# Optimization experiments

Hardware: AMD Instinct MI355X
Metric: run time of the kernel (lower is better)

Reference implementation:

```python
import jax, jax.numpy as jnp
import numpy as np
import math

B, S, D = 1, 2048, 2048          # batch, seq_len, hidden_size
H, HD = 16, 128                  # attention heads, head_dim
HV, R, NV, K = 4, 128, 2048, 4   # inner value heads, retrieval dim, num_inner_values, values per head


def rotate_half(x):
    x1, x2 = x[..., :x.shape[-1] // 2], x[..., x.shape[-1] // 2:]
    return jnp.concatenate((-x2, x1), axis=-1)


def setup_inputs() -> dict:
    key = jax.random.key(0)
    ks = jax.random.split(key, 8)
    hidden_states = jax.random.normal(ks[0], (B, S, D), jnp.float32)
    attention_mask = jnp.ones((B, S), jnp.float32)
    # standard RoPE tables, shape [B, S, HD]
    inv_freq = 1.0 / (10000.0 ** (jnp.arange(0, HD, 2, dtype=jnp.float32) / HD))
    freqs = jnp.outer(jnp.arange(S, dtype=jnp.float32), inv_freq)
    emb = jnp.concatenate((freqs, freqs), axis=-1)
    cos = jnp.broadcast_to(jnp.cos(emb)[None], (B, S, HD))
    sin = jnp.broadcast_to(jnp.sin(emb)[None], (B, S, HD))
    # learned per-head dynamic mask (binary, like torch.round init)
    dynamic_mask = jnp.round(jax.random.uniform(ks[1], (H, S), jnp.float32))
    sc = 0.02
    Wq = jax.random.normal(ks[2], (D, D), jnp.float32) * sc
    Wk = jax.random.normal(ks[3], (D, D), jnp.float32) * sc
    Wvq = jax.random.normal(ks[4], (D, HV * R), jnp.float32) * sc
    v_keys = jax.random.normal(ks[5], (HV, R, NV), jnp.float32) * sc
    v_embed = jax.random.normal(ks[6], (NV, D), jnp.float32) * sc
    Wo = jax.random.normal(ks[7], (D, D), jnp.float32) * sc
    return dict(hidden_states=hidden_states, attention_mask=attention_mask,
                cos=cos, sin=sin, dynamic_mask=dynamic_mask,
                Wq=Wq, Wk=Wk, Wvq=Wvq, v_keys=v_keys, v_embed=v_embed, Wo=Wo)


def reference(hidden_states, attention_mask, cos, sin, dynamic_mask,
              Wq, Wk, Wvq, v_keys, v_embed, Wo):
    b, s, d = hidden_states.shape
    q = hidden_states @ Wq
    k = hidden_states @ Wk
    # ---- inner_func: product-key style value retrieval ----
    vq = (hidden_states @ Wvq).reshape(b, s, HV, R).transpose(0, 2, 1, 3)  # [b,HV,s,R]
    sim = jnp.einsum('bhsr,hrn->bhsn', vq, v_keys)                         # [b,HV,s,NV]
    _, idx = jax.lax.top_k(sim, K)                                         # [b,HV,s,K]
    ve = v_embed[idx]                                                      # [b,HV,s,K,d]
    v = hidden_states * ve.sum(axis=3).sum(axis=1)                         # [b,s,d]
    # ---- heads ----
    q = q.reshape(b, s, H, HD).transpose(0, 2, 1, 3)
    k = k.reshape(b, s, H, HD).transpose(0, 2, 1, 3)
    v = v.reshape(b, s, H, HD).transpose(0, 2, 1, 3)
    # NOTE: original code rotates ONLY q (k is never rotated) -- kept faithfully
    cu, su = cos[:, None], sin[:, None]                                    # [b,1,s,HD]
    q = q * cu + rotate_half(q) * su
    attn = jnp.einsum('bhqd,bhkd->bhqk', q, k) / math.sqrt(HD)
    # ---- causal mask fused with per-head dynamic mask ----
    min_v = jnp.finfo(attn.dtype).min
    i = jnp.arange(s)
    causal = jnp.where(i[None, :] > i[:, None], min_v, 0.0).astype(attn.dtype)   # [s,s]
    causal = jnp.broadcast_to(causal[None, None], (b, H, s, s))
    am = attention_mask[:, None, None, :] * dynamic_mask[None, :, None, :s]      # [b,H,1,s]
    mask = jnp.where(causal + am == 0, min_v, causal)
    p = jax.nn.softmax(attn + mask, axis=-1)
    out = jnp.einsum('bhqk,bhkd->bhqd', p, v)
    out = out.transpose(0, 2, 1, 3).reshape(b, s, d)
    return out @ Wo
```

## Files before the change

kernel.cpp:

```cpp
#include <hip/hip_runtime.h>
#include <float.h>

#define NEG_MIN (-3.4028234663852886e38f)
#define INV_SQRT_HD 0.08838834764831845f
#define SCALE_L2E 0.12751791437968458f

typedef __attribute__((ext_vector_type(8))) short bf16x8;
typedef __attribute__((ext_vector_type(8))) unsigned short u16x8;
typedef __attribute__((ext_vector_type(4))) float f32x4;

__device__ __forceinline__ void gload_lds16(const void* g, void* l) {
  __builtin_amdgcn_global_load_lds((const __attribute__((address_space(1))) void*)g,
                                   (__attribute__((address_space(3))) void*)l, 16, 0, 0);
}
__device__ __forceinline__ ushort f2bf(float x) {
  union { float f; unsigned u; } v; v.f = x;
  unsigned r = v.u + 0x7fffu + ((v.u >> 16) & 1u);
  return (ushort)(r >> 16);
}
__device__ __forceinline__ float bf2f(ushort u) {
  union { unsigned i; float f; } v; v.i = ((unsigned)u) << 16; return v.f;
}
template<int CTRL>
__device__ __forceinline__ float dpp_ror(float x) {
  return __int_as_float(__builtin_amdgcn_mov_dpp(__float_as_int(x), CTRL, 0xF, 0xF, true));
}
template<int CTRL>
__device__ __forceinline__ unsigned dpp_ror_u(unsigned x) {
  return (unsigned)__builtin_amdgcn_mov_dpp((int)x, CTRL, 0xF, 0xF, true);
}
__device__ __forceinline__ unsigned wave_umax64(unsigned x) {
  x = max(x, dpp_ror_u<0x121>(x));
  x = max(x, dpp_ror_u<0x122>(x));
  x = max(x, dpp_ror_u<0x124>(x));
  x = max(x, dpp_ror_u<0x128>(x));
  x = max(x, (unsigned)__shfl_xor((int)x, 16));
  x = max(x, (unsigned)__shfl_xor((int)x, 32));
  return x;
}
__device__ __forceinline__ unsigned bf_sortable(ushort b) {
  return (b & 0x8000u) ? (unsigned)(b ^ 0xFFFFu) : (unsigned)(b | 0x8000u);
}

__global__ __launch_bounds__(256) void gemm_f32_sk(
    const float* __restrict__ A, int lda,
    const float* __restrict__ B, int ldb,
    float* __restrict__ Cp, int ldc, int M, int N, int Kchunk)
{
  __shared__ float As[16][132];
  __shared__ float Bs[16][132];
  const int t = threadIdx.x, tx = t & 15, ty = t >> 4;
  const int bm = blockIdx.y << 7, bn = blockIdx.x << 7;
  const int k0base = blockIdx.z * Kchunk;
  const int arr = t >> 2, ac = (t & 3) << 2;
  const int brr = t >> 5, bc = (t & 31) << 2;

  float acc[8][8];
#pragma unroll
  for (int i = 0; i < 8; ++i)
#pragma unroll
    for (int j = 0; j < 8; ++j) acc[i][j] = 0.f;

  float4 pa0, pa1, pb0, pb1;
  pa0 = *(const float4*)(A + (size_t)(bm + arr) * lda + k0base + ac);
  pa1 = *(const float4*)(A + (size_t)(bm + arr + 64) * lda + k0base + ac);
  pb0 = *(const float4*)(B + (size_t)(k0base + brr) * ldb + bn + bc);
  pb1 = *(const float4*)(B + (size_t)(k0base + brr + 8) * ldb + bn + bc);

  for (int k0 = 0; k0 < Kchunk; k0 += 16) {
    __syncthreads();
    As[ac + 0][arr] = pa0.x; As[ac + 1][arr] = pa0.y;
    As[ac + 2][arr] = pa0.z; As[ac + 3][arr] = pa0.w;
    As[ac + 0][arr + 64] = pa1.x; As[ac + 1][arr + 64] = pa1.y;
    As[ac + 2][arr + 64] = pa1.z; As[ac + 3][arr + 64] = pa1.w;
    *(float4*)(&Bs[brr][bc])     = pb0;
    *(float4*)(&Bs[brr + 8][bc]) = pb1;
    __syncthreads();
    if (k0 + 16 < Kchunk) {
      int kn = k0base + k0 + 16;
      pa0 = *(const float4*)(A + (size_t)(bm + arr) * lda + kn + ac);
      pa1 = *(const float4*)(A + (size_t)(bm + arr + 64) * lda + kn + ac);
      pb0 = *(const float4*)(B + (size_t)(kn + brr) * ldb + bn + bc);
      pb1 = *(const float4*)(B + (size_t)(kn + brr + 8) * ldb + bn + bc);
    }
#pragma unroll
    for (int kk = 0; kk < 16; ++kk) {
      float4 a0 = *(const float4*)(&As[kk][ty * 8]);
      float4 a1 = *(const float4*)(&As[kk][ty * 8 + 4]);
      float4 b0 = *(const float4*)(&Bs[kk][tx * 4]);
      float4 b1 = *(const float4*)(&Bs[kk][tx * 4 + 64]);
      float av[8] = {a0.x, a0.y, a0.z, a0.w, a1.x, a1.y, a1.z, a1.w};
      float bv[8] = {b0.x, b0.y, b0.z, b0.w, b1.x, b1.y, b1.z, b1.w};
#pragma unroll
      for (int i = 0; i < 8; ++i)
#pragma unroll
        for (int j = 0; j < 8; ++j)
          acc[i][j] = fmaf(av[i], bv[j], acc[i][j]);
    }
  }
  float* C = Cp + (size_t)blockIdx.z * M * N;
#pragma unroll
  for (int i = 0; i < 8; ++i) {
    int row = bm + ty * 8 + i;
    *(float4*)(C + (size_t)row * ldc + bn + tx * 4) =
        make_float4(acc[i][0], acc[i][1], acc[i][2], acc[i][3]);
    *(float4*)(C + (size_t)row * ldc + bn + tx * 4 + 64) =
        make_float4(acc[i][4], acc[i][5], acc[i][6], acc[i][7]);
  }
}

__global__ __launch_bounds__(256) void reduce16_cvt(const float* __restrict__ Cp,
    float* __restrict__ vq, ushort* __restrict__ vq_bf)
{
  int i = (blockIdx.x * 256 + threadIdx.x) << 2;
  float4 s = make_float4(0.f, 0.f, 0.f, 0.f);
#pragma unroll
  for (int z = 0; z < 16; ++z) {
    float4 a = *(const float4*)(Cp + (size_t)z * 1048576 + i);
    s.x += a.x; s.y += a.y; s.z += a.z; s.w += a.w;
  }
  *(float4*)(vq + i) = s;
  ushort4 o; o.x = f2bf(s.x); o.y = f2bf(s.y); o.z = f2bf(s.z); o.w = f2bf(s.w);
  *(ushort4*)(vq_bf + i) = o;
}

template<int OUT_BF16, int ROPE>
__global__ __launch_bounds__(256) void gemm_bf16(
    const ushort* __restrict__ A0, int lda,
    const ushort* __restrict__ Bt0, int ldb,
    void* __restrict__ C0, int ldc, int Kd,
    size_t strA, size_t strB, size_t strC,
    const float* __restrict__ cosb, const float* __restrict__ sinb)
{
  const ushort* A  = A0  + blockIdx.z * strA;
  const ushort* Bt = Bt0 + blockIdx.z * strB;
  __shared__ ushort smem_g[2 * 128 * 64];
  ushort* As = smem_g;
  ushort* Bs = smem_g + 128 * 64;
  const int t = threadIdx.x, w = t >> 6, lane = t & 63;
  const int lr = lane & 15, lk = lane >> 4;
  const int bm = blockIdx.y << 7, bn = blockIdx.x << 7;
  const int wm = (w >> 1) << 6, wn = (w & 1) << 6;
  f32x4 acc[4][4];
#pragma unroll
  for (int i = 0; i < 4; ++i)
#pragma unroll
    for (int j = 0; j < 4; ++j) acc[i][j] = (f32x4){0.f, 0.f, 0.f, 0.f};

  for (int k0 = 0; k0 < Kd; k0 += 64) {
    __syncthreads();
#pragma unroll
    for (int qI = 0; qI < 4; ++qI) {
      int b = w * 4096 + qI * 1024 + lane * 16;
      int row = b >> 7, colb = b & 127;
      int src = colb ^ ((row & 7) << 4);
      gload_lds16((const char*)A + ((size_t)(bm + row) * lda + k0) * 2 + src,
                  (char*)As + w * 4096 + qI * 1024);
    }
#pragma unroll
    for (int qI = 0; qI < 4; ++qI) {
      int b = w * 4096 + qI * 1024 + lane * 16;
      int row = b >> 7, colb = b & 127;
      int src = colb ^ ((row & 7) << 4);
      gload_lds16((const char*)Bt + ((size_t)(bn + row) * ldb + k0) * 2 + src,
                  (char*)Bs + w * 4096 + qI * 1024);
    }
    __syncthreads();
#pragma unroll
    for (int kk = 0; kk < 2; ++kk) {
      bf16x8 af[4], bf[4];
#pragma unroll
      for (int mi = 0; mi < 4; ++mi) {
        int row = wm + mi * 16 + lr;
        af[mi] = *(const bf16x8*)((const char*)As + row * 128 + ((kk * 64 + lk * 16) ^ ((row & 7) << 4)));
      }
#pragma unroll
      for (int ni = 0; ni < 4; ++ni) {
        int row = wn + ni * 16 + lr;
        bf[ni] = *(const bf16x8*)((const char*)Bs + row * 128 + ((kk * 64 + lk * 16) ^ ((row & 7) << 4)));
      }
#pragma unroll
      for (int mi = 0; mi < 4; ++mi)
#pragma unroll
        for (int ni = 0; ni < 4; ++ni)
          acc[mi][ni] = __builtin_amdgcn_mfma_f32_16x16x32_bf16(af[mi], bf[ni], acc[mi][ni], 0, 0, 0);
    }
  }

  if (ROPE && blockIdx.x < 16) {
    __syncthreads();
    ushort* Pl = smem_g;
#pragma unroll
    for (int mi = 0; mi < 4; ++mi)
#pragma unroll
      for (int j = 0; j < 4; ++j) {
        int rl = wm + mi * 16 + lk * 4 + j;
#pragma unroll
        for (int ni = 0; ni < 4; ++ni)
          Pl[rl * 128 + wn + ni * 16 + lr] = f2bf(acc[mi][ni][j]);
      }
    __syncthreads();
    const bool lo = (wn == 0);
#pragma unroll
    for (int mi = 0; mi < 4; ++mi)
#pragma unroll
      for (int j = 0; j < 4; ++j) {
        int rl = wm + mi * 16 + lk * 4 + j;
        int row = bm + rl;
#pragma unroll
        for (int ni = 0; ni < 4; ++ni) {
          int d = wn + ni * 16 + lr;
          float a = bf2f(Pl[rl * 128 + d]);
          float b = bf2f(Pl[rl * 128 + (d ^ 64)]);
          float cs = cosb[row * 128 + d], sn = sinb[row * 128 + d];
          float v = lo ? (a * cs - b * sn) : (a * cs + b * sn);
          ((ushort*)C0)[(size_t)row * ldc + bn + d] = f2bf(v);
        }
      }
    return;
  }

#pragma unroll
  for (int mi = 0; mi < 4; ++mi)
#pragma unroll
    for (int j = 0; j < 4; ++j) {
      int row = bm + wm + mi * 16 + lk * 4 + j;
#pragma unroll
      for (int ni = 0; ni < 4; ++ni) {
        int col = bn + wn + ni * 16 + lr;
        if (OUT_BF16) ((ushort*)C0)[blockIdx.z * strC + (size_t)row * ldc + col] = f2bf(acc[mi][ni][j]);
        else          ((float*)C0)[blockIdx.z * strC + (size_t)row * ldc + col]  = acc[mi][ni][j];
      }
    }
}

__global__ __launch_bounds__(256) void transpose_cvt_vk(
    const float* __restrict__ src0, ushort* __restrict__ dstb,
    float* __restrict__ dstf)
{
  const float* src = src0 + (size_t)blockIdx.z * 262144;
  ushort* db = dstb + (size_t)blockIdx.z * 262144;
  float*  df = dstf + (size_t)blockIdx.z * 262144;
  __shared__ float tile[64][65];
  const int r0 = blockIdx.y << 6, c0 = blockIdx.x << 6;
  const int t = threadIdx.x;
  for (int i = t; i < 1024; i += 256) {
    int r = i >> 4, c = (i & 15) << 2;
    float4 v = *(const float4*)(src + (size_t)(r0 + r) * 2048 + c0 + c);
    tile[r][c] = v.x; tile[r][c+1] = v.y; tile[r][c+2] = v.z; tile[r][c+3] = v.w;
  }
  __syncthreads();
  int c = t >> 2, rb = (t & 3) << 4;
#pragma unroll
  for (int u = 0; u < 16; u += 4) {
    float4 f = make_float4(tile[rb+u+0][c], tile[rb+u+1][c],
                           tile[rb+u+2][c], tile[rb+u+3][c]);
    ushort4 o; o.x = f2bf(f.x); o.y = f2bf(f.y); o.z = f2bf(f.z); o.w = f2bf(f.w);
    *(ushort4*)(db + (size_t)(c0 + c) * 128 + r0 + rb + u) = o;
    *(float4*) (df + (size_t)(c0 + c) * 128 + r0 + rb + u) = f;
  }
}

__global__ __launch_bounds__(256) void transpose_cvt_w3(
    const float* __restrict__ srcA, const float* __restrict__ srcB,
    const float* __restrict__ srcC, ushort* __restrict__ dst0)
{
  const float* src = (blockIdx.z == 0) ? srcA : (blockIdx.z == 1) ? srcB : srcC;
  ushort* dst = dst0 + (size_t)blockIdx.z * 4194304;
  __shared__ float tile[64][65];
  const int r0 = blockIdx.y << 6, c0 = blockIdx.x << 6;
  const int t = threadIdx.x;
  for (int i = t; i < 1024; i += 256) {
    int r = i >> 4, c = (i & 15) << 2;
    float4 v = *(const float4*)(src + (size_t)(r0 + r) * 2048 + c0 + c);
    tile[r][c] = v.x; tile[r][c+1] = v.y; tile[r][c+2] = v.z; tile[r][c+3] = v.w;
  }
  __syncthreads();
  int c = t >> 2, rb = (t & 3) << 4;
#pragma unroll
  for (int u = 0; u < 16; u += 4) {
    ushort4 o;
    o.x = f2bf(tile[rb+u+0][c]); o.y = f2bf(tile[rb+u+1][c]);
    o.z = f2bf(tile[rb+u+2][c]); o.w = f2bf(tile[rb+u+3][c]);
    *(ushort4*)(dst + (size_t)(c0 + c) * 2048 + r0 + rb + u) = o;
  }
}

__global__ __launch_bounds__(256) void transpose_bf(
    const ushort* __restrict__ src, ushort* __restrict__ dst)
{
  __shared__ ushort tile[64][66];
  const int r0 = blockIdx.y << 6, c0 = blockIdx.x << 6;
  const int t = threadIdx.x;
  for (int i = t; i < 512; i += 256) {
    int r = i >> 3, c8 = (i & 7) << 3;
    *(u16x8*)(&tile[r][c8]) = *(const u16x8*)(src + (size_t)(r0 + r) * 2048 + c0 + c8);
  }
  __syncthreads();
  for (int i = t; i < 512; i += 256) {
    int c = i >> 3, r8 = (i & 7) << 3;
    u16x8 o;
#pragma unroll
    for (int u = 0; u < 8; ++u) o[u] = tile[r8 + u][c];
    *(u16x8*)(dst + (size_t)(c0 + c) * 2048 + r0 + r8) = o;
  }
}

__global__ __launch_bounds__(256) void cvt2_bf16(const float* __restrict__ srcA,
    ushort* __restrict__ dstA, const float* __restrict__ srcB,
    ushort* __restrict__ dstB)
{
  int gid = blockIdx.x * 256 + threadIdx.x;
  const float* s; ushort* d; int i;
  if (gid < 1048576) { s = srcA; d = dstA; i = gid; }
  else               { s = srcB; d = dstB; i = gid - 1048576; }
  float4 v = ((const float4*)s)[i];
  ushort4 o; o.x = f2bf(v.x); o.y = f2bf(v.y); o.z = f2bf(v.z); o.w = f2bf(v.w);
  ((ushort4*)d)[i] = o;
}

__global__ __launch_bounds__(256) void topk_sel(const ushort* __restrict__ sim,
    const float* __restrict__ vq, const float* __restrict__ vkTf,
    int* __restrict__ idxo)
{
  const int row = blockIdx.x * 4 + (threadIdx.x >> 6);
  const int hv = row >> 11, s = row & 2047;
  const int lane = threadIdx.x & 63;
  const ushort* r = sim + (size_t)row * 2048;

  unsigned v[8];
#pragma unroll
  for (int p = 0; p < 8; ++p) v[p] = 0u;
  for (int j = 0; j < 4; ++j) {
    int nb = (lane + (j << 6)) << 3;
    u16x8 e = *(const u16x8*)(r + nb);
#pragma unroll
    for (int u = 0; u < 8; ++u) {
      unsigned pk = (bf_sortable(e[u]) << 16) | (unsigned)(2047 - (nb + u));
      if (pk > v[7]) {
        v[7] = pk;
#pragma unroll
        for (int p = 7; p > 0; --p)
          if (v[p] > v[p-1]) { unsigned tt = v[p]; v[p] = v[p-1]; v[p-1] = tt; }
      }
    }
  }
  int out_n[8];
#pragma unroll
  for (int r8 = 0; r8 < 8; ++r8) {
    unsigned m = wave_umax64(v[0]);
    out_n[r8] = 2047 - (int)(m & 0x7FFu);
    if (v[0] == m) {
#pragma unroll
      for (int p = 0; p < 7; ++p) v[p] = v[p+1];
      v[7] = 0u;
    }
  }
  const int c = lane & 7, rc = lane >> 3;
  int n = 0;
#pragma unroll
  for (int p = 0; p < 8; ++p) if (p == c) n = out_n[p];
  const float* vqr = vq + (size_t)s * 512 + hv * 128 + rc * 16;
  const float* vkf = vkTf + (size_t)hv * 262144 + (size_t)n * 128 + rc * 16;
  float acc = 0.f;
#pragma unroll
  for (int u = 0; u < 16; ++u) acc = fmaf(vqr[u], vkf[u], acc);
  acc += __shfl_xor(acc, 8);
  acc += __shfl_xor(acc, 16);
  acc += __shfl_xor(acc, 32);
  float cv = acc; int ci = n;
  int picks[4];
#pragma unroll
  for (int p = 0; p < 4; ++p) {
    float bv = cv; int bi = ci;
#pragma unroll
    for (int d = 1; d < 8; d <<= 1) {
      float ov = __shfl_xor(bv, d); int oi = __shfl_xor(bi, d);
      if (ov > bv || (ov == bv && oi < bi)) { bv = ov; bi = oi; }
    }
    picks[p] = bi;
    if (bi == ci) cv = -FLT_MAX;
  }
  if (lane == 0) {
#pragma unroll
    for (int p = 0; p < 4; ++p) idxo[(size_t)row * 4 + p] = picks[p];
  }
}

__global__ __launch_bounds__(256) void gather_mul_bf(const float* __restrict__ hs,
    const ushort* __restrict__ vemb_bf, const int* __restrict__ idx,
    ushort* __restrict__ vb)
{
  const int s = blockIdx.x;
  const int t = threadIdx.x;
  __shared__ int id[16];
  if (t < 16) id[t] = idx[((size_t)(t >> 2) * 2048 + s) * 4 + (t & 3)];
  __syncthreads();
  int d0 = t << 3;
  float g[8] = {0.f, 0.f, 0.f, 0.f, 0.f, 0.f, 0.f, 0.f};
#pragma unroll
  for (int e = 0; e < 16; ++e) {
    u16x8 ve = *(const u16x8*)(vemb_bf + (size_t)id[e] * 2048 + d0);
#pragma unroll
    for (int u = 0; u < 8; ++u) g[u] += bf2f(ve[u]);
  }
  float4 h0 = *(const float4*)(hs + (size_t)s * 2048 + d0);
  float4 h1 = *(const float4*)(hs + (size_t)s * 2048 + d0 + 4);
  float hv[8] = {h0.x, h0.y, h0.z, h0.w, h1.x, h1.y, h1.z, h1.w};
  u16x8 o;
#pragma unroll
  for (int u = 0; u < 8; ++u) o[u] = f2bf(hv[u] * g[u]);
  *(u16x8*)(vb + (size_t)s * 2048 + d0) = o;
}

__global__ __launch_bounds__(256) void vmean_part(const ushort* __restrict__ vb,
                                                  float* __restrict__ part)
{
  const int h = blockIdx.y, chunk = blockIdx.x;
  const int t = threadIdx.x, d = t & 127, half = t >> 7;
  float s = 0.f;
  int r0 = chunk * 256 + half * 128;
  for (int r = r0; r < r0 + 128; ++r)
    s += bf2f(vb[(size_t)r * 2048 + h * 128 + d]);
  __shared__ float red[256];
  red[t] = s;
  __syncthreads();
  if (t < 128) part[(size_t)(h * 8 + chunk) * 128 + d] = red[t] + red[t + 128];
}

__global__ __launch_bounds__(256) void vmean_i0(const float* __restrict__ part,
    const float* __restrict__ amask, const float* __restrict__ dmask,
    float* __restrict__ vmean, int* __restrict__ i0)
{
  const int h = blockIdx.x, t = threadIdx.x;
  if (t < 128) {
    float s = 0.f;
#pragma unroll
    for (int c = 0; c < 8; ++c) s += part[(size_t)(h * 8 + c) * 128 + t];
    vmean[h * 128 + t] = s * (1.f / 2048.f);
  }
  int best = 0x7fffffff;
  for (int j = t; j < 2048; j += 256) {
    if (amask[j] * dmask[h * 2048 + j] != 0.f) { best = j; break; }
  }
  __shared__ int red[256];
  red[t] = best;
  __syncthreads();
  for (int off = 128; off > 0; off >>= 1) {
    if (t < off) red[t] = min(red[t], red[t + off]);
    __syncthreads();
  }
  if (t == 0) i0[h] = red[0];
}

#define QLD 4096
__global__ __launch_bounds__(512) void attn_mfma(
    const ushort* __restrict__ qb, const ushort* __restrict__ kb,
    const ushort* __restrict__ vt, const float* __restrict__ amask,
    const float* __restrict__ dmask, const float* __restrict__ vmean,
    const int* __restrict__ i0, ushort* __restrict__ ao)
{
  const int L  = blockIdx.x;
  const int pr = L >> 4;
  const int h  = (L & 7) | (((L >> 3) & 1) << 3);
  const int t  = threadIdx.x, w = t >> 6, lane = t & 63;
  const int g  = w >> 2, wg = w & 3;
  const int lr = lane & 15, lk = lane >> 4;

  __shared__ char smem[155648];
  float* accL  = (float*)smem;
  float* smv   = (float*)(smem + 33792);
  float* slv   = (float*)(smem + 33792 + 512);
  float* maddL = (float*)(smem + 147456);

  const int i0h = i0[h];

  bf16x8 onesb;
#pragma unroll
  for (int u = 0; u < 8; ++u) onesb[u] = (short)0x3F80;

  for (int j = t; j < 2048; j += 512)
    maddL[j] = (amask[j] * dmask[h * 2048 + j] == 0.f) ? NEG_MIN : 0.f;

  for (int sp = 0; sp < 2; ++sp) {
    const int stripe = (sp == 0) ? pr : 31 - pr;
    const int q0 = stripe << 6;
    const int ntiles = stripe + 1;

    __syncthreads();

    const int qrow = q0 + wg * 16 + lr;
    bf16x8 qf[4];
#pragma unroll
    for (int kk = 0; kk < 4; ++kk)
      qf[kk] = *(const bf16x8*)(qb + (size_t)qrow * QLD + h * 128 + kk * 32 + lk * 8);

    if (g < ntiles) {
      const int c0 = g << 6;
#pragma unroll
      for (int qI = 0; qI < 4; ++qI) {
        int b = wg * 4096 + qI * 1024 + lane * 16;
        int row = b >> 8, colb = b & 255;
        int src = colb ^ ((row & 7) << 4);
        gload_lds16((const char*)kb + ((size_t)(c0 + row) * QLD + h * 128) * 2 + src,
                    smem + g * 32768 + b);
      }
#pragma unroll
      for (int qI = 0; qI < 4; ++qI) {
        int b = wg * 4096 + qI * 1024 + lane * 16;
        int row = b >> 7, colb = b & 127;
        int src = colb ^ ((row & 7) << 4);
        gload_lds16((const char*)vt + ((size_t)(h * 128 + row) * 2048 + c0) * 2 + src,
                    smem + 65536 + g * 32768 + b);
      }
    }

    float m[4];
    f32x4 acc_l = (f32x4){0.f, 0.f, 0.f, 0.f};
    f32x4 acc_o[8];
#pragma unroll
    for (int j = 0; j < 4; ++j) m[j] = -FLT_MAX;
#pragma unroll
    for (int ni = 0; ni < 8; ++ni) acc_o[ni] = (f32x4){0.f, 0.f, 0.f, 0.f};

    int cur = 0;
    const int niter = (ntiles + 1) >> 1;
    for (int it = 0; it < niter; ++it) {
      const int tile = 2 * it + g;
      const int c0 = tile << 6;
      __syncthreads();

      float madd[4];
      if (tile < ntiles) {
#pragma unroll
        for (int ni = 0; ni < 4; ++ni)
          madd[ni] = maddL[c0 + ni * 16 + lr];
      }

      if (tile + 2 < ntiles) {
        const int cn = c0 + 128;
        const int nb = cur ^ 1;
#pragma unroll
        for (int qI = 0; qI < 4; ++qI) {
          int b = wg * 4096 + qI * 1024 + lane * 16;
          int row = b >> 8, colb = b & 255;
          int src = colb ^ ((row & 7) << 4);
          gload_lds16((const char*)kb + ((size_t)(cn + row) * QLD + h * 128) * 2 + src,
                      smem + g * 32768 + nb * 16384 + b);
        }
#pragma unroll
        for (int qI = 0; qI < 4; ++qI) {
          int b = wg * 4096 + qI * 1024 + lane * 16;
          int row = b >> 7, colb = b & 127;
          int src = colb ^ ((row & 7) << 4);
          gload_lds16((const char*)vt + ((size_t)(h * 128 + row) * 2048 + cn) * 2 + src,
                      smem + 65536 + g * 32768 + nb * 16384 + b);
        }
      }

      if (tile < ntiles) {
        const bool diag = (tile == stripe);
        const char* Kbase = smem + g * 32768 + cur * 16384;
        const char* Vbase = smem + 65536 + g * 32768 + cur * 16384;
        char* Pbase = smem + 131072 + g * 8192;

        f32x4 sacc[4];
#pragma unroll
        for (int ni = 0; ni < 4; ++ni) sacc[ni] = (f32x4){0.f, 0.f, 0.f, 0.f};
        __builtin_amdgcn_s_setprio(1);
#pragma unroll
        for (int kk = 0; kk < 4; ++kk) {
#pragma unroll
          for (int ni = 0; ni < 4; ++ni) {
            int krow = ni * 16 + lr;
            bf16x8 bfr = *(const bf16x8*)(Kbase + krow * 256 + ((kk * 64 + lk * 16) ^ ((krow & 7) << 4)));
            sacc[ni] = __builtin_amdgcn_mfma_f32_16x16x32_bf16(qf[kk], bfr, sacc[ni], 0, 0, 0);
          }
        }
        __builtin_amdgcn_s_setprio(0);

#pragma unroll
        for (int j = 0; j < 4; ++j) {
          int grow = q0 + wg * 16 + lk * 4 + j;
          float x[4];
#pragma unroll
          for (int ni = 0; ni < 4; ++ni) {
            float v = fmaf(sacc[ni][j], SCALE_L2E, madd[ni]);
            if (diag && c0 + ni * 16 + lr > grow) v = NEG_MIN;
            x[ni] = v;
          }
          float pm = fmaxf(fmaxf(x[0], x[1]), fmaxf(x[2], x[3]));
          if (!__all(pm <= m[j] + 16.f)) {
            float tmax = pm;
            tmax = fmaxf(tmax, dpp_ror<0x121>(tmax));
            tmax = fmaxf(tmax, dpp_ror<0x122>(tmax));
            tmax = fmaxf(tmax, dpp_ror<0x124>(tmax));
            tmax = fmaxf(tmax, dpp_ror<0x128>(tmax));
            float mn = fmaxf(m[j], tmax);
            if (mn > m[j]) {
              float sc = exp2f(m[j] - mn);
              acc_l[j] *= sc;
#pragma unroll
              for (int ni = 0; ni < 8; ++ni) acc_o[ni][j] *= sc;
              m[j] = mn;
            }
          }
          int prow = wg * 16 + lk * 4 + j;
#pragma unroll
          for (int ni = 0; ni < 4; ++ni) {
            float p = exp2f(x[ni] - m[j]);
            *(ushort*)(Pbase + prow * 128 + ((2 * (ni * 16 + lr)) ^ ((prow & 7) << 4))) = f2bf(p);
          }
        }

        __builtin_amdgcn_s_setprio(1);
#pragma unroll
        for (int kk = 0; kk < 2; ++kk) {
          int prow = wg * 16 + lr;
          bf16x8 a = *(const bf16x8*)(Pbase + prow * 128 + ((kk * 64 + lk * 16) ^ ((prow & 7) << 4)));
          acc_l = __builtin_amdgcn_mfma_f32_16x16x32_bf16(a, onesb, acc_l, 0, 0, 0);
#pragma unroll
          for (int ni = 0; ni < 8; ++ni) {
            int vrow = ni * 16 + lr;
            bf16x8 bfr = *(const bf16x8*)(Vbase + vrow * 128 + ((kk * 64 + lk * 16) ^ ((vrow & 7) << 4)));
            acc_o[ni] = __builtin_amdgcn_mfma_f32_16x16x32_bf16(a, bfr, acc_o[ni], 0, 0, 0);
          }
        }
        __builtin_amdgcn_s_setprio(0);
      }
      cur ^= 1;
    }

    __syncthreads();
    if (lr == 0) {
#pragma unroll
      for (int j = 0; j < 4; ++j) {
        int r = wg * 16 + lk * 4 + j;
        smv[g * 64 + r] = m[j];
        slv[g * 64 + r] = acc_l[j];
      }
    }
    __syncthreads();
    float myf[4], lcomb[4];
#pragma unroll
    for (int j = 0; j < 4; ++j) {
      int r = wg * 16 + lk * 4 + j;
      float m0 = smv[r], m1 = smv[64 + r];
      float l0 = slv[r], l1 = slv[64 + r];
      float mm = fmaxf(m0, m1);
      float f0 = exp2f(m0 - mm), f1 = exp2f(m1 - mm);
      lcomb[j] = l0 * f0 + l1 * f1;
      myf[j] = (g == 0) ? f0 : f1;
    }
    if (g == 1) {
#pragma unroll
      for (int j = 0; j < 4; ++j) {
        int r = wg * 16 + lk * 4 + j;
#pragma unroll
        for (int ni = 0; ni < 8; ++ni)
          accL[r * 132 + ni * 16 + lr] = acc_o[ni][j] * myf[j];
      }
    }
    __syncthreads();
    if (g == 0) {
#pragma unroll
      for (int j = 0; j < 4; ++j) {
        int row = q0 + wg * 16 + lk * 4 + j;
        int r = wg * 16 + lk * 4 + j;
        if (row < i0h) {
#pragma unroll
          for (int ni = 0; ni < 8; ++ni)
            ao[(size_t)row * 2048 + h * 128 + ni * 16 + lr] = f2bf(vmean[h * 128 + ni * 16 + lr]);
        } else {
          float inv = 1.f / lcomb[j];
#pragma unroll
          for (int ni = 0; ni < 8; ++ni) {
            float o = fmaf(acc_o[ni][j], myf[j], accL[r * 132 + ni * 16 + lr]);
            ao[(size_t)row * 2048 + h * 128 + ni * 16 + lr] = f2bf(o * inv);
          }
        }
      }
    }
  }
}

extern "C" void kernel_launch(void* const* d_in, const int* in_sizes, int n_in,
                              void* d_out, int out_size, void* d_ws, size_t ws_size,
                              hipStream_t stream)
{
  const float* hs    = (const float*)d_in[0];
  const float* amask = (const float*)d_in[1];
  const float* cosb  = (const float*)d_in[2];
  const float* sinb  = (const float*)d_in[3];
  const float* dmask = (const float*)d_in[4];
  const float* Wq    = (const float*)d_in[5];
  const float* Wk    = (const float*)d_in[6];
  const float* Wvq   = (const float*)d_in[7];
  const float* vkeys = (const float*)d_in[8];
  const float* vemb  = (const float*)d_in[9];
  const float* Wo    = (const float*)d_in[10];
  float* outp = (float*)d_out;

  char* ws = (char*)d_ws;
  const size_t MB = 1048576;
  float*  pvq     = (float*) (ws + 0);
  float*  vq_f32  = (float*) (ws + 64*MB);
  ushort* vq_bf   = (ushort*)(ws + 68*MB);
  ushort* vkT     = (ushort*)(ws + 0);
  ushort* sim_bf  = (ushort*)(ws + 2*MB);
  int*    idx     = (int*)   (ws + 34*MB);
  float*  vkTf32  = (float*) (ws + 36*MB);
  ushort* vemb_bf = (ushort*)(ws + 35*MB);
  ushort* hs_bf   = (ushort*)(ws + 43*MB);
  ushort* vb      = (ushort*)(ws + 0);
  ushort* vt      = (ushort*)(ws + 8*MB);
  float*  part    = (float*) (ws + 51*MB);
  float*  vmean   = (float*) (ws + 51*MB + 65536);
  int*    i0b     = (int*)   (ws + 51*MB + 73728);
  ushort* WBig    = (ushort*)(ws + 16*MB);
  ushort* WoT     = (ushort*)(ws + 32*MB);
  ushort* qkC     = (ushort*)(ws + 52*MB);
  ushort* ao      = (ushort*)(ws + 0);

  dim3 blk(256);
  gemm_f32_sk<<<dim3(4, 16, 16), blk, 0, stream>>>(hs, 2048, Wvq, 512, pvq, 512, 2048, 512, 128);
  reduce16_cvt<<<dim3(1024), blk, 0, stream>>>(pvq, vq_f32, vq_bf);
  transpose_cvt_vk<<<dim3(32, 2, 4), blk, 0, stream>>>(vkeys, vkT, vkTf32);
  gemm_bf16<1, 0><<<dim3(16, 16, 4), blk, 0, stream>>>(vq_bf, 512, vkT, 128,
      sim_bf, 2048, 128, 128, 262144, 4194304, nullptr, nullptr);
  topk_sel<<<dim3(2048), blk, 0, stream>>>(sim_bf, vq_f32, vkTf32, idx);
  cvt2_bf16<<<dim3(8192), blk, 0, stream>>>(vemb, vemb_bf, hs, hs_bf);
  gather_mul_bf<<<dim3(2048), blk, 0, stream>>>(hs, vemb_bf, idx, vb);
  transpose_bf<<<dim3(32, 32), blk, 0, stream>>>(vb, vt);
  vmean_part<<<dim3(8, 16), blk, 0, stream>>>(vb, part);
  vmean_i0<<<dim3(16), blk, 0, stream>>>(part, amask, dmask, vmean, i0b);
  transpose_cvt_w3<<<dim3(32, 32, 3), blk, 0, stream>>>(Wq, Wk, Wo, WBig);
  gemm_bf16<1, 1><<<dim3(32, 16, 1), blk, 0, stream>>>(hs_bf, 2048, WBig, 2048,
      qkC, 4096, 2048, 0, 0, 0, cosb, sinb);
  attn_mfma<<<dim3(256), dim3(512), 0, stream>>>(qkC, qkC + 2048, vt, amask, dmask, vmean, i0b, ao);
  gemm_bf16<0, 0><<<dim3(16, 16, 1), blk, 0, stream>>>(ao, 2048, WoT, 2048,
      outp, 2048, 2048, 0, 0, 0, nullptr, nullptr);
}
```

Before: 326.0 us.

## Double-buffer LDS tiles in bf16 GEMM and halve split-K for vq projection

The bf16 MFMA GEMM now keeps two LDS buffers for the A and B tiles. It issues the global-to-LDS loads for the next K tile before computing on the current one, which removes one barrier per iteration and lets memory traffic overlap with MFMA work. The price is twice the shared memory per block (64 KB), which can lower occupancy. Separately, the f32 split-K GEMM for the vq projection uses 8 K-slices of 256 instead of 16 of 128, so the reduce kernel reads half as many partials, at the cost of fewer blocks in flight.

```diff
diff --git a/kernel.cpp b/kernel.cpp
--- a/kernel.cpp
+++ b/kernel.cpp
@@ -109,13 +109,13 @@
   }
 }
 
-__global__ __launch_bounds__(256) void reduce16_cvt(const float* __restrict__ Cp,
+__global__ __launch_bounds__(256) void reduce8_cvt(const float* __restrict__ Cp,
     float* __restrict__ vq, ushort* __restrict__ vq_bf)
 {
   int i = (blockIdx.x * 256 + threadIdx.x) << 2;
   float4 s = make_float4(0.f, 0.f, 0.f, 0.f);
 #pragma unroll
-  for (int z = 0; z < 16; ++z) {
+  for (int z = 0; z < 8; ++z) {
     float4 a = *(const float4*)(Cp + (size_t)z * 1048576 + i);
     s.x += a.x; s.y += a.y; s.z += a.z; s.w += a.w;
   }
@@ -134,9 +134,8 @@
 {
   const ushort* A  = A0  + blockIdx.z * strA;
   const ushort* Bt = Bt0 + blockIdx.z * strB;
-  __shared__ ushort smem_g[2 * 128 * 64];
-  ushort* As = smem_g;
-  ushort* Bs = smem_g + 128 * 64;
+  __shared__ ushort As[2][128 * 64];
+  __shared__ ushort Bs[2][128 * 64];
   const int t = threadIdx.x, w = t >> 6, lane = t & 63;
   const int lr = lane & 15, lk = lane >> 4;
   const int bm = blockIdx.y << 7, bn = blockIdx.x << 7;
@@ -147,37 +146,37 @@
 #pragma unroll
     for (int j = 0; j < 4; ++j) acc[i][j] = (f32x4){0.f, 0.f, 0.f, 0.f};
 
+#define STAGE_QK(buf, kk0)                                                     \
+  {                                                                            \
+_Pragma("unroll")                                                              \
+    for (int qI = 0; qI < 4; ++qI) {                                           \
+      int b = w * 4096 + qI * 1024 + lane * 16;                                \
+      int row = b >> 7, colb = b & 127;                                        \
+      int src = colb ^ ((row & 7) << 4);                                       \
+      gload_lds16((const char*)A + ((size_t)(bm + row) * lda + (kk0)) * 2 + src,\
+                  (char*)As[buf] + w * 4096 + qI * 1024);                      \
+      gload_lds16((const char*)Bt + ((size_t)(bn + row) * ldb + (kk0)) * 2 + src,\
+                  (char*)Bs[buf] + w * 4096 + qI * 1024);                      \
+    }                                                                          \
+  }
+
+  STAGE_QK(0, 0);
+  int cur = 0;
   for (int k0 = 0; k0 < Kd; k0 += 64) {
     __syncthreads();
-#pragma unroll
-    for (int qI = 0; qI < 4; ++qI) {
-      int b = w * 4096 + qI * 1024 + lane * 16;
-      int row = b >> 7, colb = b & 127;
-      int src = colb ^ ((row & 7) << 4);
-      gload_lds16((const char*)A + ((size_t)(bm + row) * lda + k0) * 2 + src,
-                  (char*)As + w * 4096 + qI * 1024);
-    }
-#pragma unroll
-    for (int qI = 0; qI < 4; ++qI) {
-      int b = w * 4096 + qI * 1024 + lane * 16;
-      int row = b >> 7, colb = b & 127;
-      int src = colb ^ ((row & 7) << 4);
-      gload_lds16((const char*)Bt + ((size_t)(bn + row) * ldb + k0) * 2 + src,
-                  (char*)Bs + w * 4096 + qI * 1024);
-    }
-    __syncthreads();
+    if (k0 + 64 < Kd) STAGE_QK(cur ^ 1, k0 + 64);
 #pragma unroll
     for (int kk = 0; kk < 2; ++kk) {
       bf16x8 af[4], bf[4];
 #pragma unroll
       for (int mi = 0; mi < 4; ++mi) {
         int row = wm + mi * 16 + lr;
-        af[mi] = *(const bf16x8*)((const char*)As + row * 128 + ((kk * 64 + lk * 16) ^ ((row & 7) << 4)));
+        af[mi] = *(const bf16x8*)((const char*)As[cur] + row * 128 + ((kk * 64 + lk * 16) ^ ((row & 7) << 4)));
       }
 #pragma unroll
       for (int ni = 0; ni < 4; ++ni) {
         int row = wn + ni * 16 + lr;
-        bf[ni] = *(const bf16x8*)((const char*)Bs + row * 128 + ((kk * 64 + lk * 16) ^ ((row & 7) << 4)));
+        bf[ni] = *(const bf16x8*)((const char*)Bs[cur] + row * 128 + ((kk * 64 + lk * 16) ^ ((row & 7) << 4)));
       }
 #pragma unroll
       for (int mi = 0; mi < 4; ++mi)
@@ -185,11 +184,13 @@
         for (int ni = 0; ni < 4; ++ni)
           acc[mi][ni] = __builtin_amdgcn_mfma_f32_16x16x32_bf16(af[mi], bf[ni], acc[mi][ni], 0, 0, 0);
     }
-  }
+    cur ^= 1;
+  }
+#undef STAGE_QK
 
   if (ROPE && blockIdx.x < 16) {
     __syncthreads();
-    ushort* Pl = smem_g;
+    ushort* Pl = (ushort*)As;
 #pragma unroll
     for (int mi = 0; mi < 4; ++mi)
 #pragma unroll
@@ -723,8 +724,8 @@
   ushort* ao      = (ushort*)(ws + 0);
 
   dim3 blk(256);
-  gemm_f32_sk<<<dim3(4, 16, 16), blk, 0, stream>>>(hs, 2048, Wvq, 512, pvq, 512, 2048, 512, 128);
-  reduce16_cvt<<<dim3(1024), blk, 0, stream>>>(pvq, vq_f32, vq_bf);
+  gemm_f32_sk<<<dim3(4, 16, 8), blk, 0, stream>>>(hs, 2048, Wvq, 512, pvq, 512, 2048, 512, 256);
+  reduce8_cvt<<<dim3(1024), blk, 0, stream>>>(pvq, vq_f32, vq_bf);
   transpose_cvt_vk<<<dim3(32, 2, 4), blk, 0, stream>>>(vkeys, vkT, vkTf32);
   gemm_bf16<1, 0><<<dim3(16, 16, 4), blk, 0, stream>>>(vq_bf, 512, vkT, 128,
       sim_bf, 2048, 128, 128, 262144, 4194304, nullptr, nullptr);
```

Result: faster. 311.5 us (-4.5%).
